# Performance work log

Measured on AMD Instinct MI355X. Metric: run time of the kernel, lower is better.

The kernel has to match this reference:

```python
import jax, jax.numpy as jnp
import numpy as np

B, C, T, H, NCLS = 512, 271, 281, 128, 1854  # batch, in_channels, seq_len, hid_dim, num_classes


def _lstm_dir(x, w_ih, w_hh, b_ih, b_hh, reverse=False):
    """Single-direction LSTM. x: [B,T,I]; w_ih: [4H,I]; w_hh: [4H,H]. Returns [B,T,H].
    PyTorch gate order: i, f, g, o."""
    Bn = x.shape[0]
    Hd = w_hh.shape[1]
    # precompute input contribution for all timesteps: [T,B,4H]
    xw = jnp.swapaxes(jnp.einsum('bti,gi->btg', x, w_ih) + b_ih, 0, 1)

    def step(carry, xw_t):
        h, c = carry
        gates = xw_t + h @ w_hh.T + b_hh
        i, f, g, o = jnp.split(gates, 4, axis=-1)
        c = jax.nn.sigmoid(f) * c + jax.nn.sigmoid(i) * jnp.tanh(g)
        h = jax.nn.sigmoid(o) * jnp.tanh(c)
        return (h, c), h

    init = (jnp.zeros((Bn, Hd), x.dtype), jnp.zeros((Bn, Hd), x.dtype))
    _, hs = jax.lax.scan(step, init, xw, reverse=reverse)  # outputs aligned to time index
    return jnp.swapaxes(hs, 0, 1)  # [B,T,H]


def setup_inputs() -> dict:
    key = jax.random.key(0)
    ks = iter(jax.random.split(key, 32))
    d = {"X": jax.random.normal(next(ks), (B, C, T), dtype=jnp.float32)}

    def u(k, shape):
        # uniform init like PyTorch LSTM: U(-1/sqrt(H), 1/sqrt(H))
        s = 1.0 / np.sqrt(H)
        return jax.random.uniform(k, shape, jnp.float32, -s, s)

    # layer 0 (input C), layer 1 (input 2H), forward/backward directions
    for l, isz in ((0, C), (1, 2 * H)):
        for dname in ('f', 'b'):
            d[f"w_ih{l}{dname}"] = u(next(ks), (4 * H, isz))
            d[f"w_hh{l}{dname}"] = u(next(ks), (4 * H, H))
            d[f"b_ih{l}{dname}"] = u(next(ks), (4 * H,))
            d[f"b_hh{l}{dname}"] = u(next(ks), (4 * H,))

    # attention params (xavier-uniform)
    lim = np.sqrt(6.0 / (2 * H + 2 * H))
    d["att_W"] = jax.random.uniform(next(ks), (2 * H, 2 * H), jnp.float32, -lim, lim)
    lim_v = np.sqrt(6.0 / (2 * H + 1))
    d["att_v"] = jax.random.uniform(next(ks), (2 * H, 1), jnp.float32, -lim_v, lim_v)
    # head
    lim_h = 1.0 / np.sqrt(2 * H)
    d["head_W"] = jax.random.uniform(next(ks), (NCLS, 2 * H), jnp.float32, -lim_h, lim_h)
    d["head_b"] = jax.random.uniform(next(ks), (NCLS,), jnp.float32, -lim_h, lim_h)
    return d


def reference(X, w_ih0f, w_hh0f, b_ih0f, b_hh0f, w_ih0b, w_hh0b, b_ih0b, b_hh0b,
              w_ih1f, w_hh1f, b_ih1f, b_hh1f, w_ih1b, w_hh1b, b_ih1b, b_hh1b,
              att_W, att_v, head_W, head_b):
    x = jnp.transpose(X, (0, 2, 1))  # [B,T,C]
    # layer 0 bidirectional
    h0 = jnp.concatenate([
        _lstm_dir(x, w_ih0f, w_hh0f, b_ih0f, b_hh0f, reverse=False),
        _lstm_dir(x, w_ih0b, w_hh0b, b_ih0b, b_hh0b, reverse=True),
    ], axis=-1)  # [B,T,2H]  (inter-layer dropout is identity in eval mode)
    # layer 1 bidirectional
    h1 = jnp.concatenate([
        _lstm_dir(h0, w_ih1f, w_hh1f, b_ih1f, b_hh1f, reverse=False),
        _lstm_dir(h0, w_ih1b, w_hh1b, b_ih1b, b_hh1b, reverse=True),
    ], axis=-1)  # [B,T,2H]
    # additive attention
    u = jnp.tanh(h1 @ att_W)                 # [B,T,2H]
    a = jnp.squeeze(u @ att_v, -1)           # [B,T]
    scores = jax.nn.softmax(a, axis=-1)
    weighted = jnp.einsum('bth,bt->bh', h1, scores)  # [B,2H]
    return weighted @ head_W.T + head_b      # [B,num_classes]
```

## Files before the change

### kernel.cpp

```cpp
#include <hip/hip_runtime.h>
#include <cstdint>
#include <cstddef>


constexpr int Bn   = 512;
constexpr int Cn   = 271;
constexpr int Tn   = 281;
constexpr int Hn   = 128;
constexpr int NCLS = 1854;
constexpr int Gn   = 4 * Hn;
constexpr int Kp0  = 288;

typedef unsigned short u16;
typedef __attribute__((__ext_vector_type__(8))) short bf16x8;
typedef __attribute__((__ext_vector_type__(4))) float f32x4;

#define DEVINL __device__ __forceinline__

DEVINL float sigm(float x)       { return 1.f / (1.f + __expf(-x)); }
DEVINL float tanhf_fast(float x) { return 2.f / (1.f + __expf(-2.f * x)) - 1.f; }

DEVINL void splitf(float v, u16& h, u16& l) {
  const uint32_t b = __float_as_uint(v);
  h = (u16)(b >> 16);
  const float lf = v - __uint_as_float(b & 0xFFFF0000u);
  l = (u16)(__float_as_uint(lf) >> 16);
}

#define GLL16(gp, lp) __builtin_amdgcn_global_load_lds(                        \
    (const __attribute__((address_space(1))) uint32_t*)(gp),                   \
    (__attribute__((address_space(3))) uint32_t*)(lp), 16, 0, 0)

template <int ACT, int NBIAS>
__global__ __launch_bounds__(256, 2) void gemm_mfma3(
    const u16* __restrict__ Ah, const u16* __restrict__ Al,
    const u16* __restrict__ Bh, const u16* __restrict__ Bl,
    const float* __restrict__ bias1, const float* __restrict__ bias2,
    float* __restrict__ Cout, int Mdim, int Ndim, int Kdim, int ldc)
{
  __shared__ __align__(16) u16 Ash[128][32];
  __shared__ __align__(16) u16 Asl[128][32];
  __shared__ __align__(16) u16 Bsh[128][32];
  __shared__ __align__(16) u16 Bsl[128][32];

  const int tid = threadIdx.x;
  const int w   = tid >> 6;
  const int l   = tid & 63;
  const int lr  = l & 15;
  const int lg  = l >> 4;
  const int row0 = blockIdx.x * 128;
  const int col0 = blockIdx.y * 128;
  const int mr = (w >> 1) * 64;
  const int nc = (w & 1) * 64;

  const f32x4 z4 = {0.f, 0.f, 0.f, 0.f};
  f32x4 acc[4][4];
#pragma unroll
  for (int m = 0; m < 4; m++)
#pragma unroll
    for (int n = 0; n < 4; n++) acc[m][n] = z4;

  const int srow  = (l >> 2);
  const int scol8 = (l & 3) * 8;

  for (int k0 = 0; k0 < Kdim; k0 += 32) {
#pragma unroll
    for (int i = 0; i < 2; i++) {
      const int lrow = w * 32 + i * 16;
      const int ra = min(row0 + lrow + srow, Mdim - 1);
      const int rb = min(col0 + lrow + srow, Ndim - 1);
      const size_t ao = (size_t)ra * Kdim + k0 + scol8;
      const size_t bo = (size_t)rb * Kdim + k0 + scol8;
      GLL16(Ah + ao, &Ash[lrow][0]);
      GLL16(Al + ao, &Asl[lrow][0]);
      GLL16(Bh + bo, &Bsh[lrow][0]);
      GLL16(Bl + bo, &Bsl[lrow][0]);
    }
    __syncthreads();

    bf16x8 afh[4], afl[4], bfh[4], bfl[4];
#pragma unroll
    for (int m = 0; m < 4; m++) {
      afh[m] = *(const bf16x8*)&Ash[mr + m * 16 + lr][lg * 8];
      afl[m] = *(const bf16x8*)&Asl[mr + m * 16 + lr][lg * 8];
    }
#pragma unroll
    for (int n = 0; n < 4; n++) {
      bfh[n] = *(const bf16x8*)&Bsh[nc + n * 16 + lr][lg * 8];
      bfl[n] = *(const bf16x8*)&Bsl[nc + n * 16 + lr][lg * 8];
    }
#pragma unroll
    for (int m = 0; m < 4; m++)
#pragma unroll
      for (int n = 0; n < 4; n++) {
        acc[m][n] = __builtin_amdgcn_mfma_f32_16x16x32_bf16(afh[m], bfh[n], acc[m][n], 0, 0, 0);
        acc[m][n] = __builtin_amdgcn_mfma_f32_16x16x32_bf16(afh[m], bfl[n], acc[m][n], 0, 0, 0);
        acc[m][n] = __builtin_amdgcn_mfma_f32_16x16x32_bf16(afl[m], bfh[n], acc[m][n], 0, 0, 0);
      }
    __syncthreads();
  }

#pragma unroll
  for (int n = 0; n < 4; n++) {
    const int gcol = col0 + nc + n * 16 + lr;
    if (gcol >= Ndim) continue;
    float bv = 0.f;
    if (NBIAS >= 1) bv += bias1[gcol];
    if (NBIAS >= 2) bv += bias2[gcol];
#pragma unroll
    for (int m = 0; m < 4; m++) {
#pragma unroll
      for (int r = 0; r < 4; r++) {
        const int grow = row0 + mr + m * 16 + lg * 4 + r;
        if (grow >= Mdim) continue;
        float v = acc[m][n][r] + bv;
        if (ACT == 1) v = tanhf_fast(v);
        Cout[(size_t)grow * ldc + gcol] = v;
      }
    }
  }
}

template <int TRANS>
__global__ __launch_bounds__(256) void split_kernel(
    const float* __restrict__ in, u16* __restrict__ oh, u16* __restrict__ ol,
    int R, int Kin, int Kout)
{
  const int r = blockIdx.x * 4 + (threadIdx.x >> 6);
  if (r >= R) return;
  const int lane = threadIdx.x & 63;
  for (int k = lane * 4; k < Kout; k += 256) {
    float v[4];
#pragma unroll
    for (int j = 0; j < 4; j++) {
      const int kk = k + j;
      v[j] = (kk < Kin)
               ? (TRANS ? in[(size_t)kk * R + r] : in[(size_t)r * Kin + kk])
               : 0.f;
    }
    u16 hs[4], ls[4];
#pragma unroll
    for (int j = 0; j < 4; j++) splitf(v[j], hs[j], ls[j]);
    const size_t o = (size_t)r * Kout + k;
    *(ushort4*)&oh[o] = make_ushort4(hs[0], hs[1], hs[2], hs[3]);
    *(ushort4*)&ol[o] = make_ushort4(ls[0], ls[1], ls[2], ls[3]);
  }
}

__global__ __launch_bounds__(256) void xsplit_kernel(
    const float* __restrict__ X, u16* __restrict__ xh, u16* __restrict__ xl)
{
  __shared__ float tile[32][33];
  const int t0 = blockIdx.x * 32, c0 = blockIdx.y * 32, b = blockIdx.z;
  const int tx = threadIdx.x & 31, ty = threadIdx.x >> 5;
#pragma unroll
  for (int i = 0; i < 4; i++) {
    const int c = c0 + ty + i * 8, t = t0 + tx;
    float v = 0.f;
    if (c < Cn && t < Tn) v = X[((size_t)b * Cn + c) * Tn + t];
    tile[ty + i * 8][tx] = v;
  }
  __syncthreads();
  const int tq = threadIdx.x >> 3;
  const int kq = (threadIdx.x & 7) * 4;
  const int t = t0 + tq;
  if (t >= Tn) return;
  u16 hs[4], ls[4];
#pragma unroll
  for (int j = 0; j < 4; j++) splitf(tile[kq + j][tq], hs[j], ls[j]);
  const size_t o = ((size_t)b * Tn + t) * Kp0 + c0 + kq;
  *(ushort4*)&xh[o] = make_ushort4(hs[0], hs[1], hs[2], hs[3]);
  *(ushort4*)&xl[o] = make_ushort4(ls[0], ls[1], ls[2], ls[3]);
}

template <int AMODE, int BMODE, int ACT, int NBIAS>
__global__ __launch_bounds__(256) void gemm_tile(
    const float* __restrict__ A, const float* __restrict__ Bm,
    const float* __restrict__ bias1, const float* __restrict__ bias2,
    float* __restrict__ Cout, int Mdim, int Ndim, int Kdim, int ldc)
{
  __shared__ __align__(16) float As[8][128];
  __shared__ __align__(16) float Bs[8][128];

  const int tid  = threadIdx.x;
  const int tx   = tid & 15;
  const int ty   = tid >> 4;
  const int row0 = blockIdx.x * 128;
  const int col0 = blockIdx.y * 128;

  float acc[8][8];
#pragma unroll
  for (int i = 0; i < 8; i++)
#pragma unroll
    for (int j = 0; j < 8; j++) acc[i][j] = 0.f;

  for (int k0 = 0; k0 < Kdim; k0 += 8) {
    if (AMODE == 0) {
      const int q  = tid >> 7;
      const int r  = tid & 127;
      const int gr = row0 + r;
      const int gk = k0 + q * 4;
      float4 v = make_float4(0.f, 0.f, 0.f, 0.f);
      if (gr < Mdim && gk + 3 < Kdim)
        v = *(const float4*)&A[(size_t)gr * Kdim + gk];
      As[q * 4 + 0][r] = v.x;
      As[q * 4 + 1][r] = v.y;
      As[q * 4 + 2][r] = v.z;
      As[q * 4 + 3][r] = v.w;
    } else {
#pragma unroll
      for (int l = 0; l < 4; l++) {
        const int e  = tid + l * 256;
        const int r  = e & 127;
        const int kk = e >> 7;
        const int gr = row0 + r;
        const int gk = k0 + kk;
        float v = 0.f;
        if (gr < Mdim && gk < Kdim) {
          const int bb = gr / Tn;
          const int tt = gr - bb * Tn;
          v = A[((size_t)bb * Cn + gk) * Tn + tt];
        }
        As[kk][r] = v;
      }
    }
#pragma unroll
    for (int l = 0; l < 4; l++) {
      const int e = tid + l * 256;
      int kk, cc;
      if (BMODE == 0) { kk = e & 7;   cc = e >> 3; }
      else            { cc = e & 127; kk = e >> 7; }
      const int gn = col0 + cc;
      const int gk = k0 + kk;
      float v = 0.f;
      if (gn < Ndim && gk < Kdim)
        v = (BMODE == 0) ? Bm[(size_t)gn * Kdim + gk]
                         : Bm[(size_t)gk * Ndim + gn];
      Bs[kk][cc] = v;
    }
    __syncthreads();
#pragma unroll
    for (int kk = 0; kk < 8; kk++) {
      const float4 a0 = *(const float4*)&As[kk][ty * 8];
      const float4 a1 = *(const float4*)&As[kk][ty * 8 + 4];
      const float4 b0 = *(const float4*)&Bs[kk][tx * 8];
      const float4 b1 = *(const float4*)&Bs[kk][tx * 8 + 4];
      const float av[8] = {a0.x, a0.y, a0.z, a0.w, a1.x, a1.y, a1.z, a1.w};
      const float bv[8] = {b0.x, b0.y, b0.z, b0.w, b1.x, b1.y, b1.z, b1.w};
#pragma unroll
      for (int i = 0; i < 8; i++)
#pragma unroll
        for (int j = 0; j < 8; j++) acc[i][j] = fmaf(av[i], bv[j], acc[i][j]);
    }
    __syncthreads();
  }
#pragma unroll
  for (int i = 0; i < 8; i++) {
    const int gr = row0 + ty * 8 + i;
    if (gr >= Mdim) continue;
    const size_t rowoff = (size_t)gr * ldc;
#pragma unroll
    for (int j = 0; j < 8; j++) {
      const int gn = col0 + tx * 8 + j;
      if (gn >= Ndim) continue;
      float v = acc[i][j];
      if (NBIAS >= 1) v += bias1[gn];
      if (NBIAS >= 2) v += bias2[gn];
      if (ACT == 1) v = tanhf_fast(v);
      Cout[rowoff + gn] = v;
    }
  }
}

__global__ __launch_bounds__(512, 1) void lstm_rec3(
    const float* __restrict__ xw,
    const float* __restrict__ whhf,
    const float* __restrict__ whhb,
    float* __restrict__ hout, int MC)
{
  const int dir = blockIdx.y;
  const int row = blockIdx.x;
  const int n   = threadIdx.x;
  const int j   = n >> 2;
  const int q   = n & 3;
  const float* __restrict__ whh = dir ? whhb : whhf;
  const float* __restrict__ xwd = xw + (size_t)dir * MC * Gn;

  __shared__ __align__(16) float hl[2][140];

  float w[4][32];
#pragma unroll
  for (int g = 0; g < 4; g++) {
    const float4* wp = (const float4*)&whh[((size_t)(g * Hn + j)) * Hn + 32 * q];
#pragma unroll
    for (int i = 0; i < 8; i++) {
      const float4 v = wp[i];
      w[g][4 * i + 0] = v.x; w[g][4 * i + 1] = v.y;
      w[g][4 * i + 2] = v.z; w[g][4 * i + 3] = v.w;
    }
  }
  if (n < 140) hl[0][n] = 0.f;
  float c = 0.f;
  float hbuf[8];
  const size_t srow = (size_t)row * Tn;
  float* __restrict__ hop = hout + srow * 256 + dir * Hn + j;
  const int jpad = j + ((j >> 5) << 2);

  float xg = xwd[(srow + (dir ? (Tn - 1) : 0)) * Gn + q * Hn + j];
  __syncthreads();

  for (int s8 = 0; s8 < Tn - 1; s8 += 8) {
#pragma unroll
    for (int u = 0; u < 8; u++) {
      const int s = s8 + u;
      const int p = u & 1;
      const int tn_ = dir ? (Tn - 2 - s) : (s + 1);
      const float xgn = xwd[(srow + tn_) * Gn + q * Hn + j];
      float a0 = 0.f, a1 = 0.f, a2 = 0.f, a3 = 0.f;
      const float* hs = &hl[p][36 * q];
#pragma unroll
      for (int i = 0; i < 8; i++) {
        const float4 h4 = *(const float4*)&hs[4 * i];
        a0 = fmaf(w[0][4 * i + 0], h4.x, a0);
        a0 = fmaf(w[0][4 * i + 1], h4.y, a0);
        a0 = fmaf(w[0][4 * i + 2], h4.z, a0);
        a0 = fmaf(w[0][4 * i + 3], h4.w, a0);
        a1 = fmaf(w[1][4 * i + 0], h4.x, a1);
        a1 = fmaf(w[1][4 * i + 1], h4.y, a1);
        a1 = fmaf(w[1][4 * i + 2], h4.z, a1);
        a1 = fmaf(w[1][4 * i + 3], h4.w, a1);
        a2 = fmaf(w[2][4 * i + 0], h4.x, a2);
        a2 = fmaf(w[2][4 * i + 1], h4.y, a2);
        a2 = fmaf(w[2][4 * i + 2], h4.z, a2);
        a2 = fmaf(w[2][4 * i + 3], h4.w, a2);
        a3 = fmaf(w[3][4 * i + 0], h4.x, a3);
        a3 = fmaf(w[3][4 * i + 1], h4.y, a3);
        a3 = fmaf(w[3][4 * i + 2], h4.z, a3);
        a3 = fmaf(w[3][4 * i + 3], h4.w, a3);
      }
      a0 += (q == 0) ? xg : 0.f;
      a1 += (q == 1) ? xg : 0.f;
      a2 += (q == 2) ? xg : 0.f;
      a3 += (q == 3) ? xg : 0.f;
      a0 += __shfl_xor(a0, 1); a0 += __shfl_xor(a0, 2);
      a1 += __shfl_xor(a1, 1); a1 += __shfl_xor(a1, 2);
      a2 += __shfl_xor(a2, 1); a2 += __shfl_xor(a2, 2);
      a3 += __shfl_xor(a3, 1); a3 += __shfl_xor(a3, 2);
      const float iv = sigm(a0);
      const float fv = sigm(a1);
      const float gv = tanhf_fast(a2);
      const float ov = sigm(a3);
      c = fv * c + iv * gv;
      const float hv = ov * tanhf_fast(c);
      if (q == 0) hl[p ^ 1][jpad] = hv;
      hbuf[u] = hv;
      __syncthreads();
      xg = xgn;
    }
    if (q == 0) {
#pragma unroll
      for (int u = 0; u < 8; u++) {
        const int ss = s8 + u;
        const int tt = dir ? (Tn - 1 - ss) : ss;
        hop[(size_t)tt * 256] = hbuf[u];
      }
    }
  }
  {
    float a0 = 0.f, a1 = 0.f, a2 = 0.f, a3 = 0.f;
    const float* hs = &hl[0][36 * q];
#pragma unroll
    for (int i = 0; i < 8; i++) {
      const float4 h4 = *(const float4*)&hs[4 * i];
      a0 = fmaf(w[0][4 * i + 0], h4.x, a0);
      a0 = fmaf(w[0][4 * i + 1], h4.y, a0);
      a0 = fmaf(w[0][4 * i + 2], h4.z, a0);
      a0 = fmaf(w[0][4 * i + 3], h4.w, a0);
      a1 = fmaf(w[1][4 * i + 0], h4.x, a1);
      a1 = fmaf(w[1][4 * i + 1], h4.y, a1);
      a1 = fmaf(w[1][4 * i + 2], h4.z, a1);
      a1 = fmaf(w[1][4 * i + 3], h4.w, a1);
      a2 = fmaf(w[2][4 * i + 0], h4.x, a2);
      a2 = fmaf(w[2][4 * i + 1], h4.y, a2);
      a2 = fmaf(w[2][4 * i + 2], h4.z, a2);
      a2 = fmaf(w[2][4 * i + 3], h4.w, a2);
      a3 = fmaf(w[3][4 * i + 0], h4.x, a3);
      a3 = fmaf(w[3][4 * i + 1], h4.y, a3);
      a3 = fmaf(w[3][4 * i + 2], h4.z, a3);
      a3 = fmaf(w[3][4 * i + 3], h4.w, a3);
    }
    a0 += (q == 0) ? xg : 0.f;
    a1 += (q == 1) ? xg : 0.f;
    a2 += (q == 2) ? xg : 0.f;
    a3 += (q == 3) ? xg : 0.f;
    a0 += __shfl_xor(a0, 1); a0 += __shfl_xor(a0, 2);
    a1 += __shfl_xor(a1, 1); a1 += __shfl_xor(a1, 2);
    a2 += __shfl_xor(a2, 1); a2 += __shfl_xor(a2, 2);
    a3 += __shfl_xor(a3, 1); a3 += __shfl_xor(a3, 2);
    const float iv = sigm(a0);
    const float fv = sigm(a1);
    const float gv = tanhf_fast(a2);
    const float ov = sigm(a3);
    c = fv * c + iv * gv;
    const float hv = ov * tanhf_fast(c);
    if (q == 0) {
      const int tt = dir ? 0 : (Tn - 1);
      hop[(size_t)tt * 256] = hv;
    }
  }
}

__global__ __launch_bounds__(256) void dot_v_kernel(
    const float* __restrict__ u, const float* __restrict__ v,
    float* __restrict__ a, int MC)
{
  const int lane = threadIdx.x & 63;
  const int row  = blockIdx.x * 4 + (threadIdx.x >> 6);
  if (row >= MC) return;
  const float4 uv = ((const float4*)(u + (size_t)row * 256))[lane];
  const float4 vv = ((const float4*)v)[lane];
  float p = uv.x * vv.x + uv.y * vv.y + uv.z * vv.z + uv.w * vv.w;
#pragma unroll
  for (int off = 32; off > 0; off >>= 1) p += __shfl_down(p, off);
  if (lane == 0) a[row] = p;
}

__global__ __launch_bounds__(256) void attn_pool(
    const float* __restrict__ a, const float* __restrict__ h1,
    float* __restrict__ wout)
{
  const int b    = blockIdx.x;
  const int tid  = threadIdx.x;
  const int lane = tid & 63;
  const int wid  = tid >> 6;
  __shared__ float sa[Tn];
  __shared__ float red[8];

  float lmax = -3.4e38f;
  for (int t = tid; t < Tn; t += 256) {
    const float x = a[(size_t)b * Tn + t];
    sa[t] = x;
    lmax  = fmaxf(lmax, x);
  }
#pragma unroll
  for (int off = 1; off < 64; off <<= 1) lmax = fmaxf(lmax, __shfl_xor(lmax, off));
  if (lane == 0) red[wid] = lmax;
  __syncthreads();
  const float bmax = fmaxf(fmaxf(red[0], red[1]), fmaxf(red[2], red[3]));

  float lsum = 0.f;
  for (int t = tid; t < Tn; t += 256) {
    const float e = __expf(sa[t] - bmax);
    sa[t] = e;
    lsum += e;
  }
#pragma unroll
  for (int off = 1; off < 64; off <<= 1) lsum += __shfl_xor(lsum, off);
  if (lane == 0) red[4 + wid] = lsum;
  __syncthreads();
  const float inv = 1.f / (red[4] + red[5] + red[6] + red[7]);

  float acc = 0.f;
  const float* hb = h1 + (size_t)b * Tn * 256 + tid;
  for (int t = 0; t < Tn; t++) acc += sa[t] * hb[(size_t)t * 256];
  wout[(size_t)b * 256 + tid] = acc * inv;
}

extern "C" void kernel_launch(void* const* d_in, const int* in_sizes, int n_in,
                              void* d_out, int out_size, void* d_ws, size_t ws_size,
                              hipStream_t stream)
{
  const float* X      = (const float*)d_in[0];
  const float* w_ih0f = (const float*)d_in[1];
  const float* w_hh0f = (const float*)d_in[2];
  const float* b_ih0f = (const float*)d_in[3];
  const float* b_hh0f = (const float*)d_in[4];
  const float* w_ih0b = (const float*)d_in[5];
  const float* w_hh0b = (const float*)d_in[6];
  const float* b_ih0b = (const float*)d_in[7];
  const float* b_hh0b = (const float*)d_in[8];
  const float* w_ih1f = (const float*)d_in[9];
  const float* w_hh1f = (const float*)d_in[10];
  const float* b_ih1f = (const float*)d_in[11];
  const float* b_hh1f = (const float*)d_in[12];
  const float* w_ih1b = (const float*)d_in[13];
  const float* w_hh1b = (const float*)d_in[14];
  const float* b_ih1b = (const float*)d_in[15];
  const float* b_hh1b = (const float*)d_in[16];
  const float* att_W  = (const float*)d_in[17];
  const float* att_v  = (const float*)d_in[18];
  const float* head_W = (const float*)d_in[19];
  const float* head_b = (const float*)d_in[20];

  auto al256 = [](size_t x) { return (x + 255) & ~(size_t)255; };

  auto need_for = [&](size_t mc) -> size_t {
    size_t s = 0;
    s += al256((size_t)512 * 256 * 4);
    s += 4 * al256((size_t)512 * Kp0 * 2);
    s += 4 * al256((size_t)512 * 256 * 2);
    s += 2 * al256((size_t)256 * 256 * 2);
    s += al256(2 * mc * (size_t)Gn * 4);
    s += al256(mc * 256 * 4);
    s += al256(mc * 256 * 4);
    s += al256(mc * 4);
    s += al256(2 * mc * (size_t)Kp0 * 2);
    return s;
  };

  int Bc = 8;
  {
    const int cands[7] = {512, 256, 128, 64, 32, 16, 8};
    for (int i = 0; i < 7; i++) {
      if (need_for((size_t)cands[i] * Tn) <= ws_size) { Bc = cands[i]; break; }
    }
  }
  const size_t MCs = (size_t)Bc * Tn;
  const int    MC  = (int)MCs;

  char* p = (char*)d_ws;
  float* wgt  = (float*)p;  p += al256((size_t)512 * 256 * 4);
  u16* w0fh = (u16*)p;      p += al256((size_t)512 * Kp0 * 2);
  u16* w0fl = (u16*)p;      p += al256((size_t)512 * Kp0 * 2);
  u16* w0bh = (u16*)p;      p += al256((size_t)512 * Kp0 * 2);
  u16* w0bl = (u16*)p;      p += al256((size_t)512 * Kp0 * 2);
  u16* w1fh = (u16*)p;      p += al256((size_t)512 * 256 * 2);
  u16* w1fl = (u16*)p;      p += al256((size_t)512 * 256 * 2);
  u16* w1bh = (u16*)p;      p += al256((size_t)512 * 256 * 2);
  u16* w1bl = (u16*)p;      p += al256((size_t)512 * 256 * 2);
  u16* aWh  = (u16*)p;      p += al256((size_t)256 * 256 * 2);
  u16* aWl  = (u16*)p;      p += al256((size_t)256 * 256 * 2);
  float* xwc = (float*)p;   p += al256(2 * MCs * (size_t)Gn * 4);
  float* h0c = (float*)p;   p += al256(MCs * 256 * 4);
  float* h1c = (float*)p;   p += al256(MCs * 256 * 4);
  float* ac  = (float*)p;   p += al256(MCs * 4);
  u16* act_h = (u16*)p;
  u16* act_l = (u16*)(p + MCs * (size_t)Kp0 * 2);
  float* u   = xwc;

  const dim3 blk(256);
  const int  mt  = (MC + 127) / 128;
  const int  nch = Bn / Bc;

  split_kernel<0><<<dim3(128), blk, 0, stream>>>(w_ih0f, w0fh, w0fl, 512, Cn, Kp0);
  split_kernel<0><<<dim3(128), blk, 0, stream>>>(w_ih0b, w0bh, w0bl, 512, Cn, Kp0);
  split_kernel<0><<<dim3(128), blk, 0, stream>>>(w_ih1f, w1fh, w1fl, 512, 256, 256);
  split_kernel<0><<<dim3(128), blk, 0, stream>>>(w_ih1b, w1bh, w1bl, 512, 256, 256);
  split_kernel<1><<<dim3(64),  blk, 0, stream>>>(att_W,  aWh,  aWl,  256, 256, 256);

  for (int ch = 0; ch < nch; ch++) {
    const float* Xc   = X + (size_t)ch * Bc * Cn * Tn;
    float*       wgtc = wgt + (size_t)ch * Bc * 256;

    xsplit_kernel<<<dim3(9, 9, Bc), blk, 0, stream>>>(Xc, act_h, act_l);
    gemm_mfma3<0, 2><<<dim3(mt, 4), blk, 0, stream>>>(
        act_h, act_l, w0fh, w0fl, b_ih0f, b_hh0f, xwc, MC, Gn, Kp0, Gn);
    gemm_mfma3<0, 2><<<dim3(mt, 4), blk, 0, stream>>>(
        act_h, act_l, w0bh, w0bl, b_ih0b, b_hh0b, xwc + MCs * Gn, MC, Gn, Kp0, Gn);
    lstm_rec3<<<dim3(Bc, 2), dim3(512), 0, stream>>>(xwc, w_hh0f, w_hh0b, h0c, MC);
    split_kernel<0><<<dim3((MC + 3) / 4), blk, 0, stream>>>(h0c, act_h, act_l, MC, 256, 256);
    gemm_mfma3<0, 2><<<dim3(mt, 4), blk, 0, stream>>>(
        act_h, act_l, w1fh, w1fl, b_ih1f, b_hh1f, xwc, MC, Gn, 256, Gn);
    gemm_mfma3<0, 2><<<dim3(mt, 4), blk, 0, stream>>>(
        act_h, act_l, w1bh, w1bl, b_ih1b, b_hh1b, xwc + MCs * Gn, MC, Gn, 256, Gn);
    lstm_rec3<<<dim3(Bc, 2), dim3(512), 0, stream>>>(xwc, w_hh1f, w_hh1b, h1c, MC);
    split_kernel<0><<<dim3((MC + 3) / 4), blk, 0, stream>>>(h1c, act_h, act_l, MC, 256, 256);
    gemm_mfma3<1, 0><<<dim3(mt, 2), blk, 0, stream>>>(
        act_h, act_l, aWh, aWl, nullptr, nullptr, u, MC, 256, 256, 256);
    dot_v_kernel<<<dim3((MC + 3) / 4), blk, 0, stream>>>(u, att_v, ac, MC);
    attn_pool<<<dim3(Bc), blk, 0, stream>>>(ac, h1c, wgtc);
  }
  gemm_tile<0, 0, 0, 1><<<dim3((Bn + 127) / 128, (NCLS + 127) / 128), blk, 0, stream>>>(
      wgt, head_W, head_b, nullptr, (float*)d_out, Bn, NCLS, 256, NCLS);
}
```

Baseline: 3.285 ms.

## Process four batch rows per recurrent block with shared-memory W_hh

The LSTM recurrence kernel now handles four sequences per 1024-thread block instead of one per 512-thread block. Each thread covers a 64-wide slice of all four gates, so the reduction needs one shuffle instead of two. The i and f gate weights are staged in LDS, while the g and o weights are read through the cache from global memory instead of sitting in registers. This amortises weight storage and per-step barriers across four rows and frees registers, at the cost of more LDS and global loads inside the serial time loop and a quarter as many blocks.

```diff
diff --git a/kernel.cpp b/kernel.cpp
--- a/kernel.cpp
+++ b/kernel.cpp
@@ -272,41 +272,50 @@
   }
 }
 
-__global__ __launch_bounds__(512, 1) void lstm_rec3(
+__global__
+__attribute__((amdgpu_flat_work_group_size(1024, 1024), amdgpu_waves_per_eu(1, 4)))
+void lstm_rec6(
     const float* __restrict__ xw,
     const float* __restrict__ whhf,
     const float* __restrict__ whhb,
     float* __restrict__ hout, int MC)
 {
-  const int dir = blockIdx.y;
-  const int row = blockIdx.x;
-  const int n   = threadIdx.x;
-  const int j   = n >> 2;
-  const int q   = n & 3;
+  const int dir  = blockIdx.y;
+  const int row4 = blockIdx.x * 4;
+  const int n    = threadIdx.x;
+  const int r    = n & 3;
+  const int q    = (n >> 2) & 1;
+  const int j    = n >> 3;
   const float* __restrict__ whh = dir ? whhb : whhf;
   const float* __restrict__ xwd = xw + (size_t)dir * MC * Gn;
 
-  __shared__ __align__(16) float hl[2][140];
-
-  float w[4][32];
-#pragma unroll
-  for (int g = 0; g < 4; g++) {
-    const float4* wp = (const float4*)&whh[((size_t)(g * Hn + j)) * Hn + 32 * q];
-#pragma unroll
-    for (int i = 0; i < 8; i++) {
-      const float4 v = wp[i];
-      w[g][4 * i + 0] = v.x; w[g][4 * i + 1] = v.y;
-      w[g][4 * i + 2] = v.z; w[g][4 * i + 3] = v.w;
-    }
-  }
-  if (n < 140) hl[0][n] = 0.f;
+  __shared__ __align__(16) float Wif[2][Hn][132];
+  __shared__ __align__(16) float hl2[2][4][132];
+
+#pragma unroll
+  for (int e = 0; e < 8; e++) {
+    const int d4 = n + e * 1024;
+    const int d  = d4 * 4;
+    const int g  = d >> 14;
+    const int jj = (d >> 7) & 127;
+    const int kk = d & 127;
+    const float4 v = *(const float4*)&whh[(size_t)d];
+    *(float4*)&Wif[g][jj][kk] = v;
+  }
+  for (int e = n; e < 2 * 4 * 132; e += 1024) ((float*)hl2)[e] = 0.f;
+
   float c = 0.f;
   float hbuf[8];
-  const size_t srow = (size_t)row * Tn;
+  const size_t srow = (size_t)(row4 + r) * Tn;
   float* __restrict__ hop = hout + srow * 256 + dir * Hn + j;
-  const int jpad = j + ((j >> 5) << 2);
-
-  float xg = xwd[(srow + (dir ? (Tn - 1) : 0)) * Gn + q * Hn + j];
+  const float* __restrict__ wgb = whh + (size_t)(2 * Hn + j) * Hn + 64 * q;
+  const float* __restrict__ wob = whh + (size_t)(3 * Hn + j) * Hn + 64 * q;
+  const float* __restrict__ xpa = xwd + srow * Gn + (2 * q + 0) * Hn + j;
+  const float* __restrict__ xpb = xwd + srow * Gn + (2 * q + 1) * Hn + j;
+
+  const int t0 = dir ? (Tn - 1) : 0;
+  float xga = xpa[(size_t)t0 * Gn];
+  float xgb = xpb[(size_t)t0 * Gn];
   __syncthreads();
 
   for (int s8 = 0; s8 < Tn - 1; s8 += 8) {
@@ -315,47 +324,49 @@
       const int s = s8 + u;
       const int p = u & 1;
       const int tn_ = dir ? (Tn - 2 - s) : (s + 1);
-      const float xgn = xwd[(srow + tn_) * Gn + q * Hn + j];
+      const float xan = xpa[(size_t)tn_ * Gn];
+      const float xbn = xpb[(size_t)tn_ * Gn];
+      int z = 0; asm volatile("" : "+v"(z));
+      const float* wip = &Wif[0][j][64 * q] + z;
+      const float* wfp = &Wif[1][j][64 * q] + z;
+      const float* wgp = wgb + z;
+      const float* wop = wob + z;
+      const float* hs  = &hl2[p][r][64 * q];
       float a0 = 0.f, a1 = 0.f, a2 = 0.f, a3 = 0.f;
-      const float* hs = &hl[p][36 * q];
-#pragma unroll
-      for (int i = 0; i < 8; i++) {
+#pragma unroll
+      for (int i = 0; i < 16; i++) {
         const float4 h4 = *(const float4*)&hs[4 * i];
-        a0 = fmaf(w[0][4 * i + 0], h4.x, a0);
-        a0 = fmaf(w[0][4 * i + 1], h4.y, a0);
-        a0 = fmaf(w[0][4 * i + 2], h4.z, a0);
-        a0 = fmaf(w[0][4 * i + 3], h4.w, a0);
-        a1 = fmaf(w[1][4 * i + 0], h4.x, a1);
-        a1 = fmaf(w[1][4 * i + 1], h4.y, a1);
-        a1 = fmaf(w[1][4 * i + 2], h4.z, a1);
-        a1 = fmaf(w[1][4 * i + 3], h4.w, a1);
-        a2 = fmaf(w[2][4 * i + 0], h4.x, a2);
-        a2 = fmaf(w[2][4 * i + 1], h4.y, a2);
-        a2 = fmaf(w[2][4 * i + 2], h4.z, a2);
-        a2 = fmaf(w[2][4 * i + 3], h4.w, a2);
-        a3 = fmaf(w[3][4 * i + 0], h4.x, a3);
-        a3 = fmaf(w[3][4 * i + 1], h4.y, a3);
-        a3 = fmaf(w[3][4 * i + 2], h4.z, a3);
-        a3 = fmaf(w[3][4 * i + 3], h4.w, a3);
+        const float4 wi = *(const float4*)&wip[4 * i];
+        const float4 wf = *(const float4*)&wfp[4 * i];
+        const float4 wg = *(const float4*)&wgp[4 * i];
+        const float4 wo = *(const float4*)&wop[4 * i];
+        a0 = fmaf(wi.x, h4.x, a0); a0 = fmaf(wi.y, h4.y, a0);
+        a0 = fmaf(wi.z, h4.z, a0); a0 = fmaf(wi.w, h4.w, a0);
+        a1 = fmaf(wf.x, h4.x, a1); a1 = fmaf(wf.y, h4.y, a1);
+        a1 = fmaf(wf.z, h4.z, a1); a1 = fmaf(wf.w, h4.w, a1);
+        a2 = fmaf(wg.x, h4.x, a2); a2 = fmaf(wg.y, h4.y, a2);
+        a2 = fmaf(wg.z, h4.z, a2); a2 = fmaf(wg.w, h4.w, a2);
+        a3 = fmaf(wo.x, h4.x, a3); a3 = fmaf(wo.y, h4.y, a3);
+        a3 = fmaf(wo.z, h4.z, a3); a3 = fmaf(wo.w, h4.w, a3);
       }
-      a0 += (q == 0) ? xg : 0.f;
-      a1 += (q == 1) ? xg : 0.f;
-      a2 += (q == 2) ? xg : 0.f;
-      a3 += (q == 3) ? xg : 0.f;
-      a0 += __shfl_xor(a0, 1); a0 += __shfl_xor(a0, 2);
-      a1 += __shfl_xor(a1, 1); a1 += __shfl_xor(a1, 2);
-      a2 += __shfl_xor(a2, 1); a2 += __shfl_xor(a2, 2);
-      a3 += __shfl_xor(a3, 1); a3 += __shfl_xor(a3, 2);
+      a0 += (q == 0) ? xga : 0.f;
+      a1 += (q == 0) ? xgb : 0.f;
+      a2 += (q == 1) ? xga : 0.f;
+      a3 += (q == 1) ? xgb : 0.f;
+      a0 += __shfl_xor(a0, 4);
+      a1 += __shfl_xor(a1, 4);
+      a2 += __shfl_xor(a2, 4);
+      a3 += __shfl_xor(a3, 4);
       const float iv = sigm(a0);
       const float fv = sigm(a1);
       const float gv = tanhf_fast(a2);
       const float ov = sigm(a3);
       c = fv * c + iv * gv;
       const float hv = ov * tanhf_fast(c);
-      if (q == 0) hl[p ^ 1][jpad] = hv;
+      if (q == 0) hl2[p ^ 1][r][j] = hv;
       hbuf[u] = hv;
       __syncthreads();
-      xg = xgn;
+      xga = xan; xgb = xbn;
     }
     if (q == 0) {
 #pragma unroll
@@ -367,36 +378,37 @@
     }
   }
   {
+    int z = 0; asm volatile("" : "+v"(z));
+    const float* wip = &Wif[0][j][64 * q] + z;
+    const float* wfp = &Wif[1][j][64 * q] + z;
+    const float* wgp = wgb + z;
+    const float* wop = wob + z;
+    const float* hs  = &hl2[0][r][64 * q];
     float a0 = 0.f, a1 = 0.f, a2 = 0.f, a3 = 0.f;
-    const float* hs = &hl[0][36 * q];
-#pragma unroll
-    for (int i = 0; i < 8; i++) {
+#pragma unroll
+    for (int i = 0; i < 16; i++) {
       const float4 h4 = *(const float4*)&hs[4 * i];
-      a0 = fmaf(w[0][4 * i + 0], h4.x, a0);
-      a0 = fmaf(w[0][4 * i + 1], h4.y, a0);
-      a0 = fmaf(w[0][4 * i + 2], h4.z, a0);
-      a0 = fmaf(w[0][4 * i + 3], h4.w, a0);
-      a1 = fmaf(w[1][4 * i + 0], h4.x, a1);
-      a1 = fmaf(w[1][4 * i + 1], h4.y, a1);
-      a1 = fmaf(w[1][4 * i + 2], h4.z, a1);
-      a1 = fmaf(w[1][4 * i + 3], h4.w, a1);
-      a2 = fmaf(w[2][4 * i + 0], h4.x, a2);
-      a2 = fmaf(w[2][4 * i + 1], h4.y, a2);
-      a2 = fmaf(w[2][4 * i + 2], h4.z, a2);
-      a2 = fmaf(w[2][4 * i + 3], h4.w, a2);
-      a3 = fmaf(w[3][4 * i + 0], h4.x, a3);
-      a3 = fmaf(w[3][4 * i + 1], h4.y, a3);
-      a3 = fmaf(w[3][4 * i + 2], h4.z, a3);
-      a3 = fmaf(w[3][4 * i + 3], h4.w, a3);
-    }
-    a0 += (q == 0) ? xg : 0.f;
-    a1 += (q == 1) ? xg : 0.f;
-    a2 += (q == 2) ? xg : 0.f;
-    a3 += (q == 3) ? xg : 0.f;
-    a0 += __shfl_xor(a0, 1); a0 += __shfl_xor(a0, 2);
-    a1 += __shfl_xor(a1, 1); a1 += __shfl_xor(a1, 2);
-    a2 += __shfl_xor(a2, 1); a2 += __shfl_xor(a2, 2);
-    a3 += __shfl_xor(a3, 1); a3 += __shfl_xor(a3, 2);
+      const float4 wi = *(const float4*)&wip[4 * i];
+      const float4 wf = *(const float4*)&wfp[4 * i];
+      const float4 wg = *(const float4*)&wgp[4 * i];
+      const float4 wo = *(const float4*)&wop[4 * i];
+      a0 = fmaf(wi.x, h4.x, a0); a0 = fmaf(wi.y, h4.y, a0);
+      a0 = fmaf(wi.z, h4.z, a0); a0 = fmaf(wi.w, h4.w, a0);
+      a1 = fmaf(wf.x, h4.x, a1); a1 = fmaf(wf.y, h4.y, a1);
+      a1 = fmaf(wf.z, h4.z, a1); a1 = fmaf(wf.w, h4.w, a1);
+      a2 = fmaf(wg.x, h4.x, a2); a2 = fmaf(wg.y, h4.y, a2);
+      a2 = fmaf(wg.z, h4.z, a2); a2 = fmaf(wg.w, h4.w, a2);
+      a3 = fmaf(wo.x, h4.x, a3); a3 = fmaf(wo.y, h4.y, a3);
+      a3 = fmaf(wo.z, h4.z, a3); a3 = fmaf(wo.w, h4.w, a3);
+    }
+    a0 += (q == 0) ? xga : 0.f;
+    a1 += (q == 0) ? xgb : 0.f;
+    a2 += (q == 1) ? xga : 0.f;
+    a3 += (q == 1) ? xgb : 0.f;
+    a0 += __shfl_xor(a0, 4);
+    a1 += __shfl_xor(a1, 4);
+    a2 += __shfl_xor(a2, 4);
+    a3 += __shfl_xor(a3, 4);
     const float iv = sigm(a0);
     const float fv = sigm(a1);
     const float gv = tanhf_fast(a2);
@@ -557,13 +569,13 @@
         act_h, act_l, w0fh, w0fl, b_ih0f, b_hh0f, xwc, MC, Gn, Kp0, Gn);
     gemm_mfma3<0, 2><<<dim3(mt, 4), blk, 0, stream>>>(
         act_h, act_l, w0bh, w0bl, b_ih0b, b_hh0b, xwc + MCs * Gn, MC, Gn, Kp0, Gn);
-    lstm_rec3<<<dim3(Bc, 2), dim3(512), 0, stream>>>(xwc, w_hh0f, w_hh0b, h0c, MC);
+    lstm_rec6<<<dim3(Bc / 4, 2), dim3(1024), 0, stream>>>(xwc, w_hh0f, w_hh0b, h0c, MC);
     split_kernel<0><<<dim3((MC + 3) / 4), blk, 0, stream>>>(h0c, act_h, act_l, MC, 256, 256);
     gemm_mfma3<0, 2><<<dim3(mt, 4), blk, 0, stream>>>(
         act_h, act_l, w1fh, w1fl, b_ih1f, b_hh1f, xwc, MC, Gn, 256, Gn);
     gemm_mfma3<0, 2><<<dim3(mt, 4), blk, 0, stream>>>(
         act_h, act_l, w1bh, w1bl, b_ih1b, b_hh1b, xwc + MCs * Gn, MC, Gn, 256, Gn);
-    lstm_rec3<<<dim3(Bc, 2), dim3(512), 0, stream>>>(xwc, w_hh1f, w_hh1b, h1c, MC);
+    lstm_rec6<<<dim3(Bc / 4, 2), dim3(1024), 0, stream>>>(xwc, w_hh1f, w_hh1b, h1c, MC);
     split_kernel<0><<<dim3((MC + 3) / 4), blk, 0, stream>>>(h1c, act_h, act_l, MC, 256, 256);
     gemm_mfma3<1, 0><<<dim3(mt, 2), blk, 0, stream>>>(
         act_h, act_l, aWh, aWl, nullptr, nullptr, u, MC, 256, 256, 256);
```

Result: slower. 7.428 ms (+126.1%).
